# Kernel optimization log

Hardware: AMD Instinct MI355X
Metric: run time of the kernel (lower is better)

The kernel has to match this reference:

```python
import jax, jax.numpy as jnp
import numpy as np

B, T, C, H = 8, 2048, 1024, 64  # batch, seq (block_size), n_embd, head_size


def setup_inputs() -> dict:
    key = jax.random.key(0)
    kx, kq, kk, kv = jax.random.split(key, 4)
    s = 1.0 / np.sqrt(C)
    return {
        "x": jax.random.normal(kx, (B, T, C), dtype=jnp.float32),
        "Wq": jax.random.normal(kq, (C, H), dtype=jnp.float32) * s,
        "Wk": jax.random.normal(kk, (C, H), dtype=jnp.float32) * s,
        "Wv": jax.random.normal(kv, (C, H), dtype=jnp.float32) * s,
    }


def reference(x, Wq, Wk, Wv):
    t = x.shape[1]
    q = jnp.einsum("btc,ch->bth", x, Wq)
    k = jnp.einsum("btc,ch->bth", x, Wk)
    v = jnp.einsum("btc,ch->bth", x, Wv)
    scores = jnp.einsum("bqh,bkh->bqk", q, k) / jnp.sqrt(jnp.float32(H))
    causal = jnp.tril(jnp.ones((t, t), dtype=bool))  # tril mask
    scores = jnp.where(causal, scores, -jnp.inf)
    attn = jax.nn.softmax(scores, axis=-1)
    return jnp.einsum("bqk,bkh->bqh", attn, v)
```

## Files before the change

kernel.cpp:

```cpp
#include <hip/hip_runtime.h>
#include <hip/hip_bf16.h>

#define BB 8
#define TT 2048
#define CC 1024
#define HH 64
#define NSPLIT 8

typedef __attribute__((ext_vector_type(8)))  short bf16x8;
typedef __attribute__((ext_vector_type(4)))  float f32x4;
typedef __attribute__((ext_vector_type(16))) float f32x16;
typedef __attribute__((ext_vector_type(8)))  unsigned short us8;
typedef unsigned int u32;

static __device__ __forceinline__ unsigned short f2bf(float f) {
    union { float f; unsigned int u; } v; v.f = f;
    unsigned int u = v.u;
    return (unsigned short)((u + 0x7FFFu + ((u >> 16) & 1u)) >> 16);
}
static __device__ __forceinline__ float bf2f(unsigned short s) {
    union { u32 u; float f; } v; v.u = ((u32)s) << 16; return v.f;
}

__global__ __launch_bounds__(256) void prep_weights(
        const float* __restrict__ Wq, const float* __restrict__ Wk,
        const float* __restrict__ Wv, unsigned short* __restrict__ Wt) {
    __shared__ float tile[64][65];
    int w  = blockIdx.x >> 4;
    int c0 = (blockIdx.x & 15) * 64;
    const float* W = (w == 0) ? Wq : (w == 1) ? Wk : Wv;
    int li = threadIdx.x;
    {
        int c = li >> 2, h4 = (li & 3) * 16;
        const float* src = W + (size_t)(c0 + c) * HH + h4;
        #pragma unroll
        for (int i = 0; i < 4; ++i) {
            float4 v4 = *(const float4*)(src + i * 4);
            tile[c][h4 + i*4 + 0] = v4.x; tile[c][h4 + i*4 + 1] = v4.y;
            tile[c][h4 + i*4 + 2] = v4.z; tile[c][h4 + i*4 + 3] = v4.w;
        }
    }
    __syncthreads();
    float scale = (w == 0) ? 0.1803368802f : 1.0f;
    int h = li >> 2, cg = (li & 3) * 16;
    unsigned short* dst = Wt + (size_t)w * HH * CC + (size_t)h * CC + c0 + cg;
    #pragma unroll
    for (int i = 0; i < 16; ++i) dst[i] = f2bf(tile[cg + i][h] * scale);
}

__global__ __launch_bounds__(512, 4) void proj_qkv(
        const float* __restrict__ x, const unsigned short* __restrict__ Wt,
        unsigned short* __restrict__ qws, unsigned short* __restrict__ kws,
        unsigned short* __restrict__ vws) {
    __shared__ unsigned short Xs[2][32 * 64];
    __shared__ unsigned short Ws[2][192 * 64];
    int tid = threadIdx.x;
    int wv = tid >> 6, lane = tid & 63;
    int quad = (lane >> 4) & 3, lq = lane & 15;
    int mg = wv >> 2, ng = wv & 3;
    int r0 = blockIdx.x * 32;

    bool xact = tid < 256;
    int xr = tid >> 3, xg = tid & 7;
    const float* xsrc = x + (size_t)(r0 + xr) * CC + xg * 8;
    int xdst = xr * 64 + ((xg ^ (xr & 7)) * 8);
    float4 xa[2], xb[2];

    f32x4 acc[3];
    #pragma unroll
    for (int nt = 0; nt < 3; ++nt)
        #pragma unroll
        for (int i = 0; i < 4; ++i) acc[nt][i] = 0.0f;

    auto stageW = [&](int buf, int kc) {
        #pragma unroll
        for (int i = 0; i < 3; ++i) {
            int fp = tid + i * 512;
            int r = fp >> 3, pb = fp & 7, g = pb ^ (r & 7);
            const u32 __attribute__((address_space(1)))* gsrc =
                (const u32 __attribute__((address_space(1)))*)
                    (Wt + (size_t)r * CC + kc * 64 + g * 8);
            u32 __attribute__((address_space(3)))* ldst =
                (u32 __attribute__((address_space(3)))*)(&Ws[buf][fp * 8]);
            __builtin_amdgcn_global_load_lds(gsrc, ldst, 16, 0, 0);
        }
    };
    auto loadX = [&](int set, int kc) {
        xa[set] = *(const float4*)(xsrc + kc * 64);
        xb[set] = *(const float4*)(xsrc + kc * 64 + 4);
    };
    auto writeX = [&](int set, int buf) {
        unsigned short h[8];
        h[0]=f2bf(xa[set].x); h[1]=f2bf(xa[set].y);
        h[2]=f2bf(xa[set].z); h[3]=f2bf(xa[set].w);
        h[4]=f2bf(xb[set].x); h[5]=f2bf(xb[set].y);
        h[6]=f2bf(xb[set].z); h[7]=f2bf(xb[set].w);
        *(us8*)&Xs[buf][xdst] = *(const us8*)h;
    };

    if (xact) { loadX(0, 0); loadX(1, 1); }
    stageW(0, 0);
    if (xact) writeX(0, 0);

    for (int kc = 0; kc < 16; ++kc) {
        int cur = kc & 1;
        __syncthreads();
        if (kc < 15) stageW(1 - cur, kc + 1);
        if (xact && kc < 14) loadX(kc & 1, kc + 2);
        #pragma unroll
        for (int ks = 0; ks < 2; ++ks) {
            int g = ks * 4 + quad;
            int arow = mg * 16 + lq;
            bf16x8 a = *(const bf16x8*)&Xs[cur][arow * 64 + (g ^ (lq & 7)) * 8];
            bf16x8 b[3];
            #pragma unroll
            for (int nt = 0; nt < 3; ++nt) {
                int brow = ng * 48 + nt * 16 + lq;
                b[nt] = *(const bf16x8*)&Ws[cur][brow * 64 + (g ^ (lq & 7)) * 8];
            }
            #pragma unroll
            for (int nt = 0; nt < 3; ++nt)
                acc[nt] = __builtin_amdgcn_mfma_f32_16x16x32_bf16(
                    a, b[nt], acc[nt], 0, 0, 0);
        }
        if (xact && kc < 15) writeX((kc + 1) & 1, 1 - cur);
    }

    __syncthreads();
    unsigned short* Vl = (unsigned short*)Xs;
    #pragma unroll
    for (int nt = 0; nt < 3; ++nt) {
        int g = ng * 48 + nt * 16 + lq;
        #pragma unroll
        for (int i = 0; i < 4; ++i) {
            int row = mg * 16 + quad * 4 + i;
            unsigned short bv = f2bf(acc[nt][i]);
            if (g < 64)       qws[(size_t)(r0 + row) * HH + g] = bv;
            else if (g < 128) kws[(size_t)(r0 + row) * HH + (g - 64)] = bv;
            else              Vl[(g - 128) * 36 + row] = bv;
        }
    }
    __syncthreads();
    if (tid < 256) {
        int h = tid >> 2, tb = (tid & 3) * 8;
        int b = r0 >> 11, rr = r0 & (TT - 1);
        *(us8*)(vws + ((size_t)b * HH + h) * TT + rr + tb) =
            *(const us8*)&Vl[h * 36 + tb];
    }
}

__global__ __launch_bounds__(128, 3) void attn(
        const unsigned short* __restrict__ qws,
        const unsigned short* __restrict__ kws,
        const unsigned short* __restrict__ vws,
        unsigned short* __restrict__ Op, float* __restrict__ Lp) {
    __shared__ unsigned short Kt[32][72];
    __shared__ unsigned short Vt[64][40];
    __shared__ unsigned short Ps[64][40];
    int ti = blockIdx.x;
    int s  = blockIdx.y;
    int b  = blockIdx.z;
    int last = 2 * ti + 1;
    if (s > last) return;
    int tid = threadIdx.x, wv = tid >> 6, lane = tid & 63;
    int half = lane >> 5, l31 = lane & 31;

    bf16x8 qf[4];
    {
        const unsigned short* qp =
            qws + ((size_t)b * TT + ti * 64 + wv * 32 + l31) * HH + half * 8;
        #pragma unroll
        for (int ks = 0; ks < 4; ++ks) qf[ks] = *(const bf16x8*)(qp + ks * 16);
    }
    f32x16 O0, O1, Lc;
    #pragma unroll
    for (int i = 0; i < 16; ++i) { O0[i] = 0.f; O1[i] = 0.f; Lc[i] = 0.f; }
    bf16x8 ones;
    #pragma unroll
    for (int i = 0; i < 8; ++i) ones[i] = (short)0x3F80;

    for (int jc = s; jc <= last; jc += NSPLIT) {
        __syncthreads();
        #pragma unroll
        for (int i = 0; i < 2; ++i) {
            int slot = tid + i * 128;
            int r = slot >> 3, g = slot & 7;
            *(us8*)&Kt[r][g * 8] =
                *(const us8*)(kws + ((size_t)b * TT + jc * 32 + r) * HH + g * 8);
        }
        #pragma unroll
        for (int i = 0; i < 2; ++i) {
            int slot = tid + i * 128;
            int h = slot >> 2, kb = slot & 3;
            *(us8*)&Vt[h][kb * 8] =
                *(const us8*)(vws + ((size_t)b * HH + h) * TT + jc * 32 + kb * 8);
        }
        __syncthreads();
        f32x16 S;
        #pragma unroll
        for (int i = 0; i < 16; ++i) S[i] = 0.f;
        #pragma unroll
        for (int ks = 0; ks < 4; ++ks) {
            bf16x8 kf = *(const bf16x8*)&Kt[l31][ks * 16 + half * 8];
            S = __builtin_amdgcn_mfma_f32_32x32x16_bf16(qf[ks], kf, S, 0, 0, 0);
        }
        bool diag = (jc >= 2 * ti + wv);
        #pragma unroll
        for (int r = 0; r < 16; ++r) {
            int pat = (r & 3) + 8 * (r >> 2) + 4 * half;
            float p = __builtin_amdgcn_exp2f(S[r]);
            if (diag && jc * 32 + l31 > ti * 64 + wv * 32 + pat) p = 0.0f;
            Ps[wv * 32 + pat][l31] = f2bf(p);
        }
        #pragma unroll
        for (int ks = 0; ks < 2; ++ks) {
            bf16x8 pa  = *(const bf16x8*)&Ps[wv * 32 + l31][ks * 16 + half * 8];
            bf16x8 vf0 = *(const bf16x8*)&Vt[l31][ks * 16 + half * 8];
            bf16x8 vf1 = *(const bf16x8*)&Vt[32 + l31][ks * 16 + half * 8];
            O0 = __builtin_amdgcn_mfma_f32_32x32x16_bf16(pa, vf0, O0, 0, 0, 0);
            O1 = __builtin_amdgcn_mfma_f32_32x32x16_bf16(pa, vf1, O1, 0, 0, 0);
            Lc = __builtin_amdgcn_mfma_f32_32x32x16_bf16(pa, ones, Lc, 0, 0, 0);
        }
    }
    unsigned short* Ob =
        Op + (((size_t)s * BB + b) * TT + ti * 64 + wv * 32) * HH;
    #pragma unroll
    for (int r = 0; r < 16; ++r) {
        int pat = (r & 3) + 8 * (r >> 2) + 4 * half;
        Ob[(size_t)pat * HH + l31]      = f2bf(O0[r]);
        Ob[(size_t)pat * HH + 32 + l31] = f2bf(O1[r]);
    }
    if (l31 == 0) {
        #pragma unroll
        for (int r = 0; r < 16; ++r) {
            int pat = (r & 3) + 8 * (r >> 2) + 4 * half;
            Lp[((size_t)s * BB + b) * TT + ti * 64 + wv * 32 + pat] = Lc[r];
        }
    }
}

__global__ __launch_bounds__(256) void norm_out(
        const unsigned short* __restrict__ Op, const float* __restrict__ Lp,
        float* __restrict__ out) {
    int idx = blockIdx.x * 256 + threadIdx.x;
    int g = idx >> 2;
    int hseg = (idx & 3) * 16;
    int ti = (g & (TT - 1)) >> 6;
    int ns = min(2 * ti + 2, NSPLIT);
    float a[16];
    #pragma unroll
    for (int j = 0; j < 16; ++j) a[j] = 0.f;
    float Ls = 0.f;
    for (int s = 0; s < ns; ++s) {
        const unsigned short* base =
            Op + ((size_t)s * BB * TT + g) * HH + hseg;
        us8 u0 = *(const us8*)base;
        us8 u1 = *(const us8*)(base + 8);
        #pragma unroll
        for (int j = 0; j < 8; ++j) { a[j] += bf2f(u0[j]); a[8 + j] += bf2f(u1[j]); }
        Ls += Lp[(size_t)s * BB * TT + g];
    }
    float inv = 1.0f / Ls;
    float* ob = out + (size_t)g * HH + hseg;
    #pragma unroll
    for (int q = 0; q < 4; ++q) {
        float4 v = make_float4(a[q*4] * inv, a[q*4+1] * inv,
                               a[q*4+2] * inv, a[q*4+3] * inv);
        ((float4*)ob)[q] = v;
    }
}

extern "C" void kernel_launch(void* const* d_in, const int* in_sizes, int n_in,
                              void* d_out, int out_size, void* d_ws, size_t ws_size,
                              hipStream_t stream) {
    (void)in_sizes; (void)n_in; (void)out_size; (void)ws_size;
    const float* x  = (const float*)d_in[0];
    const float* Wq = (const float*)d_in[1];
    const float* Wk = (const float*)d_in[2];
    const float* Wv = (const float*)d_in[3];
    float* out = (float*)d_out;

    char* ws = (char*)d_ws;
    unsigned short* Wt  = (unsigned short*)ws;
    unsigned short* qws = (unsigned short*)(ws + (1u << 19));
    unsigned short* kws = (unsigned short*)(ws + (1u << 19) + (1u << 21));
    unsigned short* vws = (unsigned short*)(ws + (1u << 19) + (2u << 21));
    unsigned short* Op  = (unsigned short*)(ws + (1u << 19) + (3u << 21));
    float*          Lp  = (float*)(ws + (1u << 19) + (3u << 21) + (1u << 24));

    prep_weights<<<48, 256, 0, stream>>>(Wq, Wk, Wv, Wt);
    proj_qkv<<<512, 512, 0, stream>>>(x, Wt, qws, kws, vws);
    attn<<<dim3(32, NSPLIT, 8), 128, 0, stream>>>(qws, kws, vws, Op, Lp);
    norm_out<<<256, 256, 0, stream>>>(Op, Lp, out);
}
```

Before: 139.6 us.

## Split-K QKV projection with 64-row tiles and separate reduction kernel

The QKV projection now uses 64-row tiles, so each block reuses every staged weight tile across twice as many rows, and the K dimension is split in two across blockIdx.y. Each half writes bf16 partial sums to a new workspace buffer. A new qkv_reduce kernel adds the two halves, writes Q and K, and transposes V. This cuts weight traffic per row, but adds an extra launch, a global round-trip of the partials, and a second bf16 rounding of the partial sums.

```diff
diff --git a/kernel.cpp b/kernel.cpp
--- a/kernel.cpp
+++ b/kernel.cpp
@@ -50,27 +50,28 @@
 
 __global__ __launch_bounds__(512, 4) void proj_qkv(
         const float* __restrict__ x, const unsigned short* __restrict__ Wt,
-        unsigned short* __restrict__ qws, unsigned short* __restrict__ kws,
-        unsigned short* __restrict__ vws) {
-    __shared__ unsigned short Xs[2][32 * 64];
+        unsigned short* __restrict__ Pp) {
+    __shared__ unsigned short Xs[2][64 * 64];
     __shared__ unsigned short Ws[2][192 * 64];
     int tid = threadIdx.x;
     int wv = tid >> 6, lane = tid & 63;
     int quad = (lane >> 4) & 3, lq = lane & 15;
     int mg = wv >> 2, ng = wv & 3;
-    int r0 = blockIdx.x * 32;
-
-    bool xact = tid < 256;
+    int r0 = blockIdx.x * 64;
+    int k0 = blockIdx.y * 512;
+
     int xr = tid >> 3, xg = tid & 7;
-    const float* xsrc = x + (size_t)(r0 + xr) * CC + xg * 8;
+    const float* xsrc = x + (size_t)(r0 + xr) * CC + k0 + xg * 8;
     int xdst = xr * 64 + ((xg ^ (xr & 7)) * 8);
     float4 xa[2], xb[2];
 
-    f32x4 acc[3];
-    #pragma unroll
-    for (int nt = 0; nt < 3; ++nt)
-        #pragma unroll
-        for (int i = 0; i < 4; ++i) acc[nt][i] = 0.0f;
+    f32x4 acc[2][3];
+    #pragma unroll
+    for (int mt = 0; mt < 2; ++mt)
+        #pragma unroll
+        for (int nt = 0; nt < 3; ++nt)
+            #pragma unroll
+            for (int i = 0; i < 4; ++i) acc[mt][nt][i] = 0.0f;
 
     auto stageW = [&](int buf, int kc) {
         #pragma unroll
@@ -79,7 +80,7 @@
             int r = fp >> 3, pb = fp & 7, g = pb ^ (r & 7);
             const u32 __attribute__((address_space(1)))* gsrc =
                 (const u32 __attribute__((address_space(1)))*)
-                    (Wt + (size_t)r * CC + kc * 64 + g * 8);
+                    (Wt + (size_t)r * CC + k0 + kc * 64 + g * 8);
             u32 __attribute__((address_space(3)))* ldst =
                 (u32 __attribute__((address_space(3)))*)(&Ws[buf][fp * 8]);
             __builtin_amdgcn_global_load_lds(gsrc, ldst, 16, 0, 0);
@@ -98,54 +99,100 @@
         *(us8*)&Xs[buf][xdst] = *(const us8*)h;
     };
 
-    if (xact) { loadX(0, 0); loadX(1, 1); }
+    loadX(0, 0); loadX(1, 1);
     stageW(0, 0);
-    if (xact) writeX(0, 0);
-
-    for (int kc = 0; kc < 16; ++kc) {
+    writeX(0, 0);
+
+    for (int kc = 0; kc < 8; ++kc) {
         int cur = kc & 1;
         __syncthreads();
-        if (kc < 15) stageW(1 - cur, kc + 1);
-        if (xact && kc < 14) loadX(kc & 1, kc + 2);
+        if (kc < 7) stageW(1 - cur, kc + 1);
+        if (kc < 6) loadX(kc & 1, kc + 2);
         #pragma unroll
         for (int ks = 0; ks < 2; ++ks) {
             int g = ks * 4 + quad;
-            int arow = mg * 16 + lq;
-            bf16x8 a = *(const bf16x8*)&Xs[cur][arow * 64 + (g ^ (lq & 7)) * 8];
-            bf16x8 b[3];
+            bf16x8 a[2], b[3];
+            #pragma unroll
+            for (int mt = 0; mt < 2; ++mt) {
+                int arow = mg * 32 + mt * 16 + lq;
+                a[mt] = *(const bf16x8*)&Xs[cur][arow * 64 + (g ^ (lq & 7)) * 8];
+            }
             #pragma unroll
             for (int nt = 0; nt < 3; ++nt) {
                 int brow = ng * 48 + nt * 16 + lq;
                 b[nt] = *(const bf16x8*)&Ws[cur][brow * 64 + (g ^ (lq & 7)) * 8];
             }
             #pragma unroll
-            for (int nt = 0; nt < 3; ++nt)
-                acc[nt] = __builtin_amdgcn_mfma_f32_16x16x32_bf16(
-                    a, b[nt], acc[nt], 0, 0, 0);
-        }
-        if (xact && kc < 15) writeX((kc + 1) & 1, 1 - cur);
-    }
-
+            for (int mt = 0; mt < 2; ++mt)
+                #pragma unroll
+                for (int nt = 0; nt < 3; ++nt)
+                    acc[mt][nt] = __builtin_amdgcn_mfma_f32_16x16x32_bf16(
+                        a[mt], b[nt], acc[mt][nt], 0, 0, 0);
+        }
+        if (kc < 7) writeX((kc + 1) & 1, 1 - cur);
+    }
+
+    unsigned short* Pb =
+        Pp + ((size_t)blockIdx.y * (BB * TT) + r0) * 192;
+    #pragma unroll
+    for (int mt = 0; mt < 2; ++mt) {
+        #pragma unroll
+        for (int nt = 0; nt < 3; ++nt) {
+            int g = ng * 48 + nt * 16 + lq;
+            #pragma unroll
+            for (int i = 0; i < 4; ++i) {
+                int row = mg * 32 + mt * 16 + quad * 4 + i;
+                Pb[(size_t)row * 192 + g] = f2bf(acc[mt][nt][i]);
+            }
+        }
+    }
+}
+
+__global__ __launch_bounds__(256) void qkv_reduce(
+        const unsigned short* __restrict__ Pp,
+        unsigned short* __restrict__ qws, unsigned short* __restrict__ kws,
+        unsigned short* __restrict__ vws) {
+    __shared__ unsigned short Vt[64][72];
+    int t = threadIdx.x;
+    int br0 = blockIdx.x * 64;
+    const size_t H2 = (size_t)BB * TT * 192;
+    {
+        int r = br0 + (t >> 2), cg = (t & 3) * 32;
+        const unsigned short* p0 = Pp + (size_t)r * 192 + cg;
+        const unsigned short* p1 = p0 + H2;
+        unsigned short* dst = (cg < 64) ? (qws + (size_t)r * HH + cg)
+                                        : (kws + (size_t)r * HH + (cg - 64));
+        #pragma unroll
+        for (int u = 0; u < 4; ++u) {
+            us8 a = *(const us8*)(p0 + u * 8);
+            us8 b = *(const us8*)(p1 + u * 8);
+            unsigned short o[8];
+            #pragma unroll
+            for (int j = 0; j < 8; ++j) o[j] = f2bf(bf2f(a[j]) + bf2f(b[j]));
+            *(us8*)(dst + u * 8) = *(const us8*)o;
+        }
+    }
+    {
+        int r = br0 + (t >> 2), ch = (t & 3) * 16;
+        const unsigned short* p0 = Pp + (size_t)r * 192 + 128 + ch;
+        const unsigned short* p1 = p0 + H2;
+        #pragma unroll
+        for (int u = 0; u < 2; ++u) {
+            us8 a = *(const us8*)(p0 + u * 8);
+            us8 b = *(const us8*)(p1 + u * 8);
+            #pragma unroll
+            for (int j = 0; j < 8; ++j)
+                Vt[ch + u * 8 + j][r & 63] = f2bf(bf2f(a[j]) + bf2f(b[j]));
+        }
+    }
     __syncthreads();
-    unsigned short* Vl = (unsigned short*)Xs;
-    #pragma unroll
-    for (int nt = 0; nt < 3; ++nt) {
-        int g = ng * 48 + nt * 16 + lq;
-        #pragma unroll
-        for (int i = 0; i < 4; ++i) {
-            int row = mg * 16 + quad * 4 + i;
-            unsigned short bv = f2bf(acc[nt][i]);
-            if (g < 64)       qws[(size_t)(r0 + row) * HH + g] = bv;
-            else if (g < 128) kws[(size_t)(r0 + row) * HH + (g - 64)] = bv;
-            else              Vl[(g - 128) * 36 + row] = bv;
-        }
-    }
-    __syncthreads();
-    if (tid < 256) {
-        int h = tid >> 2, tb = (tid & 3) * 8;
-        int b = r0 >> 11, rr = r0 & (TT - 1);
-        *(us8*)(vws + ((size_t)b * HH + h) * TT + rr + tb) =
-            *(const us8*)&Vl[h * 36 + tb];
+    {
+        int h = t >> 2, tb = (t & 3) * 16;
+        int b = br0 >> 11, rr = br0 & (TT - 1);
+        #pragma unroll
+        for (int u = 0; u < 2; ++u)
+            *(us8*)(vws + ((size_t)b * HH + h) * TT + rr + tb + u * 8) =
+                *(const us8*)&Vt[h][tb + u * 8];
     }
 }
 
@@ -287,9 +334,12 @@
     unsigned short* vws = (unsigned short*)(ws + (1u << 19) + (2u << 21));
     unsigned short* Op  = (unsigned short*)(ws + (1u << 19) + (3u << 21));
     float*          Lp  = (float*)(ws + (1u << 19) + (3u << 21) + (1u << 24));
+    unsigned short* Pp  = (unsigned short*)(ws + (1u << 19) + (3u << 21)
+                                            + (1u << 24) + (1u << 19));
 
     prep_weights<<<48, 256, 0, stream>>>(Wq, Wk, Wv, Wt);
-    proj_qkv<<<512, 512, 0, stream>>>(x, Wt, qws, kws, vws);
+    proj_qkv<<<dim3(256, 2), 512, 0, stream>>>(x, Wt, Pp);
+    qkv_reduce<<<256, 256, 0, stream>>>(Pp, qws, kws, vws);
     attn<<<dim3(32, NSPLIT, 8), 128, 0, stream>>>(qws, kws, vws, Op, Lp);
     norm_out<<<256, 256, 0, stream>>>(Op, Lp, out);
 }
```

After: 136.9 us. No clear change (-1.9%).
